# Kernel optimization log

Hardware: AMD Instinct MI355X
Metric: run time of the kernel (lower is better)

The kernel has to match this reference:

```python
import jax, jax.numpy as jnp
import numpy as np

B, LQ, LK, D = 4, 2048, 2048, 1024
H = 16  # num_heads == num_kv_heads (only runnable config of the source module)
HD = D // H  # 64


def setup_inputs() -> dict:
    key = jax.random.key(0)
    ks = jax.random.split(key, 4)
    std = 0.02
    return {
        "x": jax.random.normal(ks[0], (B, LQ, D), dtype=jnp.float32),
        "text_input": jax.random.normal(ks[1], (B, LK, D), dtype=jnp.float32),
        "Wq": jax.random.normal(ks[2], (D, D), dtype=jnp.float32) * std,
        "bq": jnp.zeros((D,), dtype=jnp.float32),
        "Wkv": jax.random.normal(ks[3], (D, 2 * D), dtype=jnp.float32) * std,
        "bkv": jnp.zeros((2 * D,), dtype=jnp.float32),
    }


def reference(x, text_input, Wq, bq, Wkv, bkv):
    b, lq, d = x.shape
    lk = text_input.shape[1]
    # projections
    Q = x @ Wq + bq                       # [b, lq, d]
    KV = text_input @ Wkv + bkv           # [b, lk, 2d]
    K, V = jnp.split(KV, 2, axis=-1)      # [b, lk, d] each
    # split heads (num_kv_heads == num_heads, so repeat_interleave is identity)
    Q = Q.reshape(b, lq, H, HD)
    K = K.reshape(b, lk, H, HD)
    V = V.reshape(b, lk, H, HD)
    # scaled dot-product attention
    scale = 1.0 / jnp.sqrt(jnp.asarray(HD, dtype=Q.dtype))
    scores = jnp.einsum("bqhd,bkhd->bhqk", Q, K) * scale  # [b, H, lq, lk]
    attn = jax.nn.softmax(scores, axis=-1)
    out = jnp.einsum("bhqk,bkhd->bqhd", attn, V)          # [b, lq, H, HD]
    # dropout p=0.0 (eval) -> identity
    return out.reshape(b, lq, d)
```

## Files before the change

kernel.cpp:

```cpp
#include <hip/hip_runtime.h>
#include <hip/hip_bf16.h>


typedef unsigned short u16;
typedef unsigned int u32;

typedef __attribute__((ext_vector_type(8))) __bf16 bf16x8;
typedef __attribute__((ext_vector_type(2))) _Float16 f16x2;
typedef __attribute__((ext_vector_type(8))) _Float16 f16x8;
typedef __attribute__((ext_vector_type(4))) float f32x4;
typedef __attribute__((ext_vector_type(16))) float f32x16;
typedef __attribute__((ext_vector_type(4))) float f4;
typedef __attribute__((ext_vector_type(4))) unsigned short u16x4;
typedef __attribute__((ext_vector_type(4))) unsigned int u32x4;

#define DEVI __device__ __forceinline__

DEVI u16 f2b(float f) {
  u32 u = __float_as_uint(f);
  return (u16)((u + 0x7fffu + ((u >> 16) & 1u)) >> 16);
}

DEVI u16 f2h(float f) {
  _Float16 h = (_Float16)f;
  return __builtin_bit_cast(u16, h);
}

DEVI f16x2 pk_f16(float a, float b) {
  return __builtin_bit_cast(f16x2, __builtin_amdgcn_cvt_pkrtz(a, b));
}

DEVI u32 cvt_pk_bf16(float a, float b) {
  u32 r;
  asm("v_cvt_pk_bf16_f32 %0, %1, %2" : "=v"(r) : "v"(a), "v"(b));
  return r;
}

DEVI void gld_lds16(void* lds, const void* g) {
  __builtin_amdgcn_global_load_lds(
      (const __attribute__((address_space(1))) u32*)g,
      (__attribute__((address_space(3))) u32*)lds, 16, 0, 0);
}

__global__ __launch_bounds__(256) void k_prep(
    const float* __restrict__ Wq, const float* __restrict__ Wkv,
    u16* __restrict__ WQT, u16* __restrict__ WKVT) {
  __shared__ float tile[32][33];
  const int bid = blockIdx.x, tid = threadIdx.x;
  const float* in;
  u16* out;
  int N, bx, by;
  if (bid < 1024) {
    in = Wq; out = WQT; N = 1024; bx = bid & 31; by = bid >> 5;
  } else {
    int b2 = bid - 1024; in = Wkv; out = WKVT; N = 2048; bx = b2 & 63; by = b2 >> 6;
  }
  const int K = 1024;
  const int n0 = bx * 32, k0 = by * 32;
  const int tx = tid & 31, ty = tid >> 5;
#pragma unroll
  for (int j = 0; j < 32; j += 8)
    tile[ty + j][tx] = in[(size_t)(k0 + ty + j) * N + n0 + tx];
  __syncthreads();
#pragma unroll
  for (int j = 0; j < 32; j += 8)
    out[(size_t)(n0 + ty + j) * K + k0 + tx] = f2b(tile[tx][ty + j]);
}

__global__ __launch_bounds__(256) void k_gemm(
    const float* __restrict__ X, const float* __restrict__ TXT,
    const u16* __restrict__ WQT, const u16* __restrict__ WKVT,
    const float* __restrict__ bq, const float* __restrict__ bkv,
    u16* __restrict__ QG, u16* __restrict__ KG, u16* __restrict__ VG) {
  __shared__ alignas(16) char As[2][8192];
  __shared__ alignas(16) char Bs[4][8192];
  const int bid0 = blockIdx.x;
  const int bid = (bid0 & 7) * 192 + (bid0 >> 3);
  const int tid = threadIdx.x;
  const int w = tid >> 6, l = tid & 63;
  const int wr = w >> 1, wc = w & 1;

  const bool isQ = bid < 512;
  int nb, mb;
  const float* Af32;
  const u16* Bptr;
  const float* bias;
  if (isQ) {
    nb = bid & 7; mb = bid >> 3; Af32 = X; Bptr = WQT; bias = bq;
  } else {
    int b2 = bid - 512; nb = b2 & 15; mb = b2 >> 4; Af32 = TXT; Bptr = WKVT; bias = bkv;
  }
  const int m0 = mb << 7, n0 = nb << 7;

  u32 doff[2], bsoff[2], fsoff[2];
#pragma unroll
  for (int i = 0; i < 2; i++) {
    u32 o = (u32)(i * 4096 + tid * 16);
    u32 row = o >> 6;
    u32 csw = (o & 63) ^ (((row >> 1) & 3) << 4);
    doff[i] = o;
    bsoff[i] = row * 2048 + csw;
    fsoff[i] = row * 4096 + 2 * csw;
  }
  const char* Abase = (const char*)Af32 + (size_t)m0 * 4096;
  const char* Borig = (const char*)Bptr + (size_t)n0 * 2048;

  f32x16 acc[2][2];
#pragma unroll
  for (int i = 0; i < 2; i++)
#pragma unroll
    for (int j = 0; j < 2; j++)
#pragma unroll
      for (int e = 0; e < 16; e++) acc[i][j][e] = 0.f;

  const u32 xk = (u32)((l >> 1) & 3);
  const u32 hi5 = (u32)(l >> 5);
  const u32 arow0 = (u32)(wr * 64 + (l & 31)) * 64;
  const u32 brow0 = (u32)(wc * 64 + (l & 31)) * 64;

  f4 sa0[4][2], sa1[4][2];

#pragma unroll
  for (int s = 0; s < 3; s++) {
#pragma unroll
    for (int i = 0; i < 2; i++) gld_lds16(&Bs[s][doff[i]], Borig + (u32)s * 64 + bsoff[i]);
#pragma unroll
    for (int i = 0; i < 2; i++) {
      sa0[s][i] = *(const f4*)(Abase + (u32)s * 128 + fsoff[i]);
      sa1[s][i] = *(const f4*)(Abase + (u32)s * 128 + fsoff[i] + 16);
    }
  }
#pragma unroll
  for (int i = 0; i < 2; i++) {
    u32x4 pk;
    pk.x = cvt_pk_bf16(sa0[0][i].x, sa0[0][i].y);
    pk.y = cvt_pk_bf16(sa0[0][i].z, sa0[0][i].w);
    pk.z = cvt_pk_bf16(sa1[0][i].x, sa1[0][i].y);
    pk.w = cvt_pk_bf16(sa1[0][i].z, sa1[0][i].w);
    *(u32x4*)&As[0][doff[i]] = pk;
  }
  asm volatile("s_waitcnt lgkmcnt(0)" ::: "memory");
  __builtin_amdgcn_s_barrier();

#define GEMM_BODY(KT, J, P)                                                        \
  do {                                                                             \
    const int kt = (KT);                                                           \
    const int S3 = ((J) + 3) & 3;                                                  \
    const int S1 = ((J) + 1) & 3;                                                  \
    if (kt < 29) { \
      _Pragma("unroll") for (int i = 0; i < 2; i++)                                \
          gld_lds16(&Bs[S3][doff[i]], Borig + (u32)(kt + 3) * 64 + bsoff[i]);      \
      _Pragma("unroll") for (int i = 0; i < 2; i++) {                              \
        sa0[S3][i] = *(const f4*)(Abase + (u32)(kt + 3) * 128 + fsoff[i]);         \
        sa1[S3][i] = *(const f4*)(Abase + (u32)(kt + 3) * 128 + fsoff[i] + 16);    \
      }                                                                            \
    }                                                                              \
    if (kt < 31) {       \
      _Pragma("unroll") for (int i = 0; i < 2; i++) {                              \
        u32x4 pk;                                                                  \
        pk.x = cvt_pk_bf16(sa0[S1][i].x, sa0[S1][i].y);                            \
        pk.y = cvt_pk_bf16(sa0[S1][i].z, sa0[S1][i].w);                            \
        pk.z = cvt_pk_bf16(sa1[S1][i].x, sa1[S1][i].y);                            \
        pk.w = cvt_pk_bf16(sa1[S1][i].z, sa1[S1][i].w);                            \
        *(u32x4*)&As[(P) ^ 1][doff[i]] = pk;                                       \
      }                                                                            \
    }                                                                              \
    bf16x8 af[2][2], bfr[2][2];                                                    \
    _Pragma("unroll") for (int i = 0; i < 2; i++)                                  \
        _Pragma("unroll") for (int h = 0; h < 2; h++) {                            \
      const u32 co = (((u32)(2 * h) + hi5) ^ xk) << 4;                             \
      af[i][h] = *(const bf16x8*)&As[(P)][arow0 + (u32)i * 2048 + co];             \
      bfr[i][h] = *(const bf16x8*)&Bs[(J)][brow0 + (u32)i * 2048 + co];            \
    }                                                                              \
    _Pragma("unroll") for (int i = 0; i < 2; i++)                                  \
        _Pragma("unroll") for (int j2 = 0; j2 < 2; j2++)                           \
            _Pragma("unroll") for (int h = 0; h < 2; h++)                          \
                acc[i][j2] = __builtin_amdgcn_mfma_f32_32x32x16_bf16(              \
                    af[i][h], bfr[j2][h], acc[i][j2], 0, 0, 0);                    \
    asm volatile("s_waitcnt lgkmcnt(0)" ::: "memory");                             \
    __builtin_amdgcn_s_barrier();                                                  \
  } while (0)

  for (int k4 = 0; k4 < 8; k4++) {
    const int kt0 = k4 * 4;
    GEMM_BODY(kt0 + 0, 0, 0);
    GEMM_BODY(kt0 + 1, 1, 1);
    GEMM_BODY(kt0 + 2, 2, 0);
    GEMM_BODY(kt0 + 3, 3, 1);
  }
#undef GEMM_BODY

#pragma unroll
  for (int i = 0; i < 2; i++)
#pragma unroll
    for (int j = 0; j < 2; j++) {
      const int n = n0 + wc * 64 + j * 32 + (l & 31);
      const float bv = bias[n];
#pragma unroll
      for (int rg = 0; rg < 4; rg++) {
        const int mbase = m0 + wr * 64 + i * 32 + rg * 8 + ((l >> 5) << 2);
        const int bb = mbase >> 11;
        const int mrow = mbase & 2047;
        float a0 = acc[i][j][rg * 4 + 0] + bv;
        float a1 = acc[i][j][rg * 4 + 1] + bv;
        float a2 = acc[i][j][rg * 4 + 2] + bv;
        float a3 = acc[i][j][rg * 4 + 3] + bv;
        if (isQ) {
          const int h = n >> 6, hd = n & 63;
          u16* dst = QG + ((((size_t)bb * 16 + h) * 2048 + mrow) << 6) + hd;
          dst[0] = f2b(a0 * 0.18033688011112042f);
          dst[64] = f2b(a1 * 0.18033688011112042f);
          dst[128] = f2b(a2 * 0.18033688011112042f);
          dst[192] = f2b(a3 * 0.18033688011112042f);
        } else if (n < 1024) {
          const int h = n >> 6, d = n & 63;
          char* base = (char*)KG + ((((size_t)bb * 16 + h) * 2048 + mrow) << 7);
          float av[4] = {a0, a1, a2, a3};
#pragma unroll
          for (int r = 0; r < 4; r++) {
            u32 off = (u32)r * 128 + (((u32)d * 2) ^ (((u32)(mrow + r) & 7) << 4));
            *(u16*)(base + off) = f2b(av[r]);
          }
        } else {
          const int nn = n - 1024;
          const int h = nn >> 6, hd = nn & 63;
          u16x4 pk;
          pk.x = f2h(a0); pk.y = f2h(a1); pk.z = f2h(a2); pk.w = f2h(a3);
          char* base = (char*)VG + (((size_t)bb * 16 + h) << 18);
          u32 off = ((u32)(mrow >> 6) << 13) + (((u32)(mrow >> 5) & 1) << 12) +
                    ((u32)(hd >> 4) << 10) + (((u32)(mrow >> 2) & 3) << 8) +
                    ((u32)(hd & 15) << 4) + (((u32)(mrow >> 4) & 1) << 3);
          *(u16x4*)(base + off) = pk;
        }
      }
    }
}

__global__ __launch_bounds__(256) void k_attn(
    const u16* __restrict__ QG, const u16* __restrict__ KG, const u16* __restrict__ VG,
    float* __restrict__ out) {
  __shared__ alignas(16) char Ks[2][8192];
  __shared__ alignas(16) char Vs[2][8192];
  const int tid = threadIdx.x, w = tid >> 6, l = tid & 63;
  const int g = l >> 4, q = l & 15;
  const int bid = blockIdx.x;
  const int orig = (bid & 7) * 128 + (bid >> 3);
  const int qt = orig & 15;
  const int hh = (orig >> 4) & 15;
  const int b = orig >> 8;
  const size_t bh = (size_t)b * 16 + hh;

  const int qrowA = qt * 128 + w * 16 + q;
  const int qrowB = qrowA + 64;

  const u16* QpA = QG + ((bh * 2048 + (size_t)qrowA) << 6) + (g << 3);
  const u16* QpB = QG + ((bh * 2048 + (size_t)qrowB) << 6) + (g << 3);
  const bf16x8 qf0a = *(const bf16x8*)QpA;
  const bf16x8 qf1a = *(const bf16x8*)(QpA + 32);
  const bf16x8 qf0b = *(const bf16x8*)QpB;
  const bf16x8 qf1b = *(const bf16x8*)(QpB + 32);

  const char* Kbase = (const char*)KG + (bh << 18);
  const char* Vbase = (const char*)VG + (bh << 18);

  f32x4 lsA = (f32x4){0.f, 0.f, 0.f, 0.f};
  f32x4 lsB = (f32x4){0.f, 0.f, 0.f, 0.f};
  f32x4 oa[4], ob4[4];
#pragma unroll
  for (int c = 0; c < 4; c++) {
    oa[c] = (f32x4){0.f, 0.f, 0.f, 0.f};
    ob4[c] = (f32x4){0.f, 0.f, 0.f, 0.f};
  }
  f16x8 ones8;
#pragma unroll
  for (int e = 0; e < 8; e++) ones8[e] = (_Float16)1.0f;

  gld_lds16(&Ks[0][tid * 16], Kbase + tid * 16);
  gld_lds16(&Ks[0][4096 + tid * 16], Kbase + 4096 + tid * 16);
  gld_lds16(&Vs[0][tid * 16], Vbase + tid * 16);
  gld_lds16(&Vs[0][4096 + tid * 16], Vbase + 4096 + tid * 16);
  __syncthreads();

  const u32 ksw = ((u32)(l & 7)) << 4;
  const u32 kro = ((u32)q) << 7;
  const u32 kin = ((u32)g) << 4;

  auto body = [&](int BUF, int kb) {
    if (kb < 31) {
      const char* kp = Kbase + (size_t)(kb + 1) * 8192 + tid * 16;
      const char* vp = Vbase + (size_t)(kb + 1) * 8192 + tid * 16;
      gld_lds16(&Ks[BUF ^ 1][tid * 16], kp);
      gld_lds16(&Ks[BUF ^ 1][4096 + tid * 16], kp + 4096);
      gld_lds16(&Vs[BUF ^ 1][tid * 16], vp);
      gld_lds16(&Vs[BUF ^ 1][4096 + tid * 16], vp + 4096);
    }
    f32x4 sa[4], sb[4];
    __builtin_amdgcn_s_setprio(1);
#pragma unroll
    for (int t = 0; t < 4; t++) {
      const char* kr = &Ks[BUF][kro + (u32)t * 2048];
      bf16x8 kf0 = *(const bf16x8*)(kr + (kin ^ ksw));
      bf16x8 kf1 = *(const bf16x8*)(kr + ((kin + 64) ^ ksw));
      f32x4 z = (f32x4){0.f, 0.f, 0.f, 0.f};
      sa[t] = __builtin_amdgcn_mfma_f32_16x16x32_bf16(kf0, qf0a, z, 0, 0, 0);
      sa[t] = __builtin_amdgcn_mfma_f32_16x16x32_bf16(kf1, qf1a, sa[t], 0, 0, 0);
      sb[t] = __builtin_amdgcn_mfma_f32_16x16x32_bf16(kf0, qf0b, z, 0, 0, 0);
      sb[t] = __builtin_amdgcn_mfma_f32_16x16x32_bf16(kf1, qf1b, sb[t], 0, 0, 0);
    }
    __builtin_amdgcn_s_setprio(0);

    float pA[4][4], pB[4][4];
#pragma unroll
    for (int t = 0; t < 4; t++)
#pragma unroll
      for (int r = 0; r < 4; r++) {
        pA[t][r] = __builtin_amdgcn_exp2f(sa[t][r]);
        pB[t][r] = __builtin_amdgcn_exp2f(sb[t][r]);
      }

    __builtin_amdgcn_s_setprio(1);
#pragma unroll
    for (int u = 0; u < 2; u++) {
      f16x2 a0 = pk_f16(pA[2 * u][0], pA[2 * u][1]);
      f16x2 a1 = pk_f16(pA[2 * u][2], pA[2 * u][3]);
      f16x2 a2 = pk_f16(pA[2 * u + 1][0], pA[2 * u + 1][1]);
      f16x2 a3 = pk_f16(pA[2 * u + 1][2], pA[2 * u + 1][3]);
      f16x8 pfa;
      pfa[0] = a0.x; pfa[1] = a0.y; pfa[2] = a1.x; pfa[3] = a1.y;
      pfa[4] = a2.x; pfa[5] = a2.y; pfa[6] = a3.x; pfa[7] = a3.y;
      f16x2 b0 = pk_f16(pB[2 * u][0], pB[2 * u][1]);
      f16x2 b1 = pk_f16(pB[2 * u][2], pB[2 * u][3]);
      f16x2 b2 = pk_f16(pB[2 * u + 1][0], pB[2 * u + 1][1]);
      f16x2 b3 = pk_f16(pB[2 * u + 1][2], pB[2 * u + 1][3]);
      f16x8 pfb;
      pfb[0] = b0.x; pfb[1] = b0.y; pfb[2] = b1.x; pfb[3] = b1.y;
      pfb[4] = b2.x; pfb[5] = b2.y; pfb[6] = b3.x; pfb[7] = b3.y;
      lsA = __builtin_amdgcn_mfma_f32_16x16x32_f16(ones8, pfa, lsA, 0, 0, 0);
      lsB = __builtin_amdgcn_mfma_f32_16x16x32_f16(ones8, pfb, lsB, 0, 0, 0);
#pragma unroll
      for (int c = 0; c < 4; c++) {
        f16x8 vf = *(const f16x8*)&Vs[BUF][(u32)u * 4096 + (u32)c * 1024 + (u32)l * 16];
        oa[c] = __builtin_amdgcn_mfma_f32_16x16x32_f16(vf, pfa, oa[c], 0, 0, 0);
        ob4[c] = __builtin_amdgcn_mfma_f32_16x16x32_f16(vf, pfb, ob4[c], 0, 0, 0);
      }
    }
    __builtin_amdgcn_s_setprio(0);
    __syncthreads();
  };

  for (int kb2 = 0; kb2 < 16; kb2++) {
    body(0, 2 * kb2);
    body(1, 2 * kb2 + 1);
  }

  const float invA = 1.0f / lsA.x;
  const float invB = 1.0f / lsB.x;
  float* obA = out + ((size_t)b * 2048 + (size_t)qrowA) * 1024 + hh * 64;
  float* obB = out + ((size_t)b * 2048 + (size_t)qrowB) * 1024 + hh * 64;
#pragma unroll
  for (int c = 0; c < 4; c++) {
    f32x4 va = oa[c] * invA;
    f32x4 vb2 = ob4[c] * invB;
    *(f32x4*)(obA + c * 16 + g * 4) = va;
    *(f32x4*)(obB + c * 16 + g * 4) = vb2;
  }
}

extern "C" void kernel_launch(void* const* d_in, const int* in_sizes, int n_in,
                              void* d_out, int out_size, void* d_ws, size_t ws_size,
                              hipStream_t stream) {
  const float* x = (const float*)d_in[0];
  const float* text = (const float*)d_in[1];
  const float* Wq = (const float*)d_in[2];
  const float* bq = (const float*)d_in[3];
  const float* Wkv = (const float*)d_in[4];
  const float* bkv = (const float*)d_in[5];
  float* out = (float*)d_out;
  char* ws = (char*)d_ws;

  const size_t MiB = 1u << 20;
  u16* WQT = (u16*)(ws + 0 * MiB);
  u16* WKVT = (u16*)(ws + 2 * MiB);
  u16* QG = (u16*)(ws + 6 * MiB);
  u16* KG = (u16*)(ws + 22 * MiB);
  u16* VG = (u16*)(ws + 38 * MiB);

  k_prep<<<3072, 256, 0, stream>>>(Wq, Wkv, WQT, WKVT);
  k_gemm<<<1536, 256, 0, stream>>>(x, text, WQT, WKVT, bq, bkv, QG, KG, VG);
  k_attn<<<1024, 256, 0, stream>>>(QG, KG, VG, out);
}
```

Baseline: 162.7 us.

## Widen GEMM tile to 128x256 and switch to simple double buffering

The projection GEMM tile grows from 128x128 to 128x256, so each wave computes 2x4 MFMA accumulators, more work reuses each A tile, and the grid is halved to 768 blocks. The deep 4-stage B ring and 3-deep register prefetch of A are replaced by a 2-stage double buffer. Each step now waits on vmcnt(0) before its barrier, and A conversion is deferred until after the MFMAs. This aims to cut global and LDS traffic per FLOP, at the cost of shallower latency hiding, more accumulator registers (lower occupancy), and fewer blocks to spread over the CUs.

```diff
diff --git a/kernel.cpp b/kernel.cpp
--- a/kernel.cpp
+++ b/kernel.cpp
@@ -73,149 +73,155 @@
     const float* __restrict__ bq, const float* __restrict__ bkv,
     u16* __restrict__ QG, u16* __restrict__ KG, u16* __restrict__ VG) {
   __shared__ alignas(16) char As[2][8192];
-  __shared__ alignas(16) char Bs[4][8192];
+  __shared__ alignas(16) char Bs[2][16384];
   const int bid0 = blockIdx.x;
-  const int bid = (bid0 & 7) * 192 + (bid0 >> 3);
+  const int bid = (bid0 & 7) * 96 + (bid0 >> 3);
   const int tid = threadIdx.x;
   const int w = tid >> 6, l = tid & 63;
   const int wr = w >> 1, wc = w & 1;
 
-  const bool isQ = bid < 512;
+  const bool isQ = bid < 256;
   int nb, mb;
   const float* Af32;
   const u16* Bptr;
   const float* bias;
   if (isQ) {
-    nb = bid & 7; mb = bid >> 3; Af32 = X; Bptr = WQT; bias = bq;
+    nb = bid & 3; mb = bid >> 2; Af32 = X; Bptr = WQT; bias = bq;
   } else {
-    int b2 = bid - 512; nb = b2 & 15; mb = b2 >> 4; Af32 = TXT; Bptr = WKVT; bias = bkv;
-  }
-  const int m0 = mb << 7, n0 = nb << 7;
-
-  u32 doff[2], bsoff[2], fsoff[2];
+    int b2 = bid - 256; nb = b2 & 7; mb = b2 >> 3; Af32 = TXT; Bptr = WKVT; bias = bkv;
+  }
+  const int m0 = mb << 7, n0 = nb << 8;
+
+  u32 doffA[2], fsoff[2];
+  u32 doffB[4], bsoff[4];
 #pragma unroll
   for (int i = 0; i < 2; i++) {
     u32 o = (u32)(i * 4096 + tid * 16);
     u32 row = o >> 6;
     u32 csw = (o & 63) ^ (((row >> 1) & 3) << 4);
-    doff[i] = o;
-    bsoff[i] = row * 2048 + csw;
+    doffA[i] = o;
     fsoff[i] = row * 4096 + 2 * csw;
+  }
+#pragma unroll
+  for (int j = 0; j < 4; j++) {
+    u32 o = (u32)(j * 4096 + tid * 16);
+    u32 row = o >> 6;
+    u32 csw = (o & 63) ^ (((row >> 1) & 3) << 4);
+    doffB[j] = o;
+    bsoff[j] = row * 2048 + csw;
   }
   const char* Abase = (const char*)Af32 + (size_t)m0 * 4096;
   const char* Borig = (const char*)Bptr + (size_t)n0 * 2048;
 
-  f32x16 acc[2][2];
+  f32x16 acc[2][4];
 #pragma unroll
   for (int i = 0; i < 2; i++)
 #pragma unroll
-    for (int j = 0; j < 2; j++)
+    for (int j = 0; j < 4; j++)
 #pragma unroll
       for (int e = 0; e < 16; e++) acc[i][j][e] = 0.f;
 
   const u32 xk = (u32)((l >> 1) & 3);
   const u32 hi5 = (u32)(l >> 5);
   const u32 arow0 = (u32)(wr * 64 + (l & 31)) * 64;
-  const u32 brow0 = (u32)(wc * 64 + (l & 31)) * 64;
-
-  f4 sa0[4][2], sa1[4][2];
-
-#pragma unroll
-  for (int s = 0; s < 3; s++) {
-#pragma unroll
-    for (int i = 0; i < 2; i++) gld_lds16(&Bs[s][doff[i]], Borig + (u32)s * 64 + bsoff[i]);
-#pragma unroll
-    for (int i = 0; i < 2; i++) {
-      sa0[s][i] = *(const f4*)(Abase + (u32)s * 128 + fsoff[i]);
-      sa1[s][i] = *(const f4*)(Abase + (u32)s * 128 + fsoff[i] + 16);
-    }
+  const u32 brow0 = (u32)(wc * 128 + (l & 31)) * 64;
+
+  f4 a0[2], a1[2];
+
+#pragma unroll
+  for (int j = 0; j < 4; j++) gld_lds16(&Bs[0][doffB[j]], Borig + bsoff[j]);
+#pragma unroll
+  for (int i = 0; i < 2; i++) {
+    a0[i] = *(const f4*)(Abase + fsoff[i]);
+    a1[i] = *(const f4*)(Abase + fsoff[i] + 16);
   }
 #pragma unroll
   for (int i = 0; i < 2; i++) {
     u32x4 pk;
-    pk.x = cvt_pk_bf16(sa0[0][i].x, sa0[0][i].y);
-    pk.y = cvt_pk_bf16(sa0[0][i].z, sa0[0][i].w);
-    pk.z = cvt_pk_bf16(sa1[0][i].x, sa1[0][i].y);
-    pk.w = cvt_pk_bf16(sa1[0][i].z, sa1[0][i].w);
-    *(u32x4*)&As[0][doff[i]] = pk;
-  }
-  asm volatile("s_waitcnt lgkmcnt(0)" ::: "memory");
+    pk.x = cvt_pk_bf16(a0[i].x, a0[i].y);
+    pk.y = cvt_pk_bf16(a0[i].z, a0[i].w);
+    pk.z = cvt_pk_bf16(a1[i].x, a1[i].y);
+    pk.w = cvt_pk_bf16(a1[i].z, a1[i].w);
+    *(u32x4*)&As[0][doffA[i]] = pk;
+  }
+  asm volatile("s_waitcnt vmcnt(0) lgkmcnt(0)" ::: "memory");
   __builtin_amdgcn_s_barrier();
 
-#define GEMM_BODY(KT, J, P)                                                        \
+#define GEMM_BODY(KT, BUF)                                                         \
   do {                                                                             \
     const int kt = (KT);                                                           \
-    const int S3 = ((J) + 3) & 3;                                                  \
-    const int S1 = ((J) + 1) & 3;                                                  \
-    if (kt < 29) { \
-      _Pragma("unroll") for (int i = 0; i < 2; i++)                                \
-          gld_lds16(&Bs[S3][doff[i]], Borig + (u32)(kt + 3) * 64 + bsoff[i]);      \
+    if (kt < 31) {     \
+      _Pragma("unroll") for (int j = 0; j < 4; j++)                                \
+          gld_lds16(&Bs[(BUF) ^ 1][doffB[j]],                                      \
+                    Borig + (u32)(kt + 1) * 64 + bsoff[j]);                        \
       _Pragma("unroll") for (int i = 0; i < 2; i++) {                              \
-        sa0[S3][i] = *(const f4*)(Abase + (u32)(kt + 3) * 128 + fsoff[i]);         \
-        sa1[S3][i] = *(const f4*)(Abase + (u32)(kt + 3) * 128 + fsoff[i] + 16);    \
+        a0[i] = *(const f4*)(Abase + (u32)(kt + 1) * 128 + fsoff[i]);              \
+        a1[i] = *(const f4*)(Abase + (u32)(kt + 1) * 128 + fsoff[i] + 16);         \
       }                                                                            \
     }                                                                              \
-    if (kt < 31) {       \
-      _Pragma("unroll") for (int i = 0; i < 2; i++) {                              \
-        u32x4 pk;                                                                  \
-        pk.x = cvt_pk_bf16(sa0[S1][i].x, sa0[S1][i].y);                            \
-        pk.y = cvt_pk_bf16(sa0[S1][i].z, sa0[S1][i].w);                            \
-        pk.z = cvt_pk_bf16(sa1[S1][i].x, sa1[S1][i].y);                            \
-        pk.w = cvt_pk_bf16(sa1[S1][i].z, sa1[S1][i].w);                            \
-        *(u32x4*)&As[(P) ^ 1][doff[i]] = pk;                                       \
-      }                                                                            \
-    }                                                                              \
-    bf16x8 af[2][2], bfr[2][2];                                                    \
+    bf16x8 af[2][2];                                                               \
     _Pragma("unroll") for (int i = 0; i < 2; i++)                                  \
         _Pragma("unroll") for (int h = 0; h < 2; h++) {                            \
       const u32 co = (((u32)(2 * h) + hi5) ^ xk) << 4;                             \
-      af[i][h] = *(const bf16x8*)&As[(P)][arow0 + (u32)i * 2048 + co];             \
-      bfr[i][h] = *(const bf16x8*)&Bs[(J)][brow0 + (u32)i * 2048 + co];            \
+      af[i][h] = *(const bf16x8*)&As[(BUF)][arow0 + (u32)i * 2048 + co];           \
     }                                                                              \
-    _Pragma("unroll") for (int i = 0; i < 2; i++)                                  \
-        _Pragma("unroll") for (int j2 = 0; j2 < 2; j2++)                           \
-            _Pragma("unroll") for (int h = 0; h < 2; h++)                          \
-                acc[i][j2] = __builtin_amdgcn_mfma_f32_32x32x16_bf16(              \
-                    af[i][h], bfr[j2][h], acc[i][j2], 0, 0, 0);                    \
-    asm volatile("s_waitcnt lgkmcnt(0)" ::: "memory");                             \
+    _Pragma("unroll") for (int j2 = 0; j2 < 4; j2++) {                             \
+      bf16x8 bf[2];                                                                \
+      _Pragma("unroll") for (int h = 0; h < 2; h++) {                              \
+        const u32 co = (((u32)(2 * h) + hi5) ^ xk) << 4;                           \
+        bf[h] = *(const bf16x8*)&Bs[(BUF)][brow0 + (u32)j2 * 2048 + co];           \
+      }                                                                            \
+      _Pragma("unroll") for (int i = 0; i < 2; i++)                                \
+          _Pragma("unroll") for (int h = 0; h < 2; h++)                            \
+              acc[i][j2] = __builtin_amdgcn_mfma_f32_32x32x16_bf16(                \
+                  af[i][h], bf[h], acc[i][j2], 0, 0, 0);                           \
+    }                                                                              \
+    if (kt < 31) {                                \
+      _Pragma("unroll") for (int i = 0; i < 2; i++) {                              \
+        u32x4 pk;                                                                  \
+        pk.x = cvt_pk_bf16(a0[i].x, a0[i].y);                                      \
+        pk.y = cvt_pk_bf16(a0[i].z, a0[i].w);                                      \
+        pk.z = cvt_pk_bf16(a1[i].x, a1[i].y);                                      \
+        pk.w = cvt_pk_bf16(a1[i].z, a1[i].w);                                      \
+        *(u32x4*)&As[(BUF) ^ 1][doffA[i]] = pk;                                    \
+      }                                                                            \
+    }                                                                              \
+    asm volatile("s_waitcnt vmcnt(0) lgkmcnt(0)" ::: "memory");                    \
     __builtin_amdgcn_s_barrier();                                                  \
   } while (0)
 
-  for (int k4 = 0; k4 < 8; k4++) {
-    const int kt0 = k4 * 4;
-    GEMM_BODY(kt0 + 0, 0, 0);
-    GEMM_BODY(kt0 + 1, 1, 1);
-    GEMM_BODY(kt0 + 2, 2, 0);
-    GEMM_BODY(kt0 + 3, 3, 1);
+  for (int k2 = 0; k2 < 16; k2++) {
+    GEMM_BODY(2 * k2, 0);
+    GEMM_BODY(2 * k2 + 1, 1);
   }
 #undef GEMM_BODY
 
 #pragma unroll
   for (int i = 0; i < 2; i++)
 #pragma unroll
-    for (int j = 0; j < 2; j++) {
-      const int n = n0 + wc * 64 + j * 32 + (l & 31);
+    for (int j = 0; j < 4; j++) {
+      const int n = n0 + wc * 128 + j * 32 + (l & 31);
       const float bv = bias[n];
 #pragma unroll
       for (int rg = 0; rg < 4; rg++) {
         const int mbase = m0 + wr * 64 + i * 32 + rg * 8 + ((l >> 5) << 2);
         const int bb = mbase >> 11;
         const int mrow = mbase & 2047;
-        float a0 = acc[i][j][rg * 4 + 0] + bv;
-        float a1 = acc[i][j][rg * 4 + 1] + bv;
-        float a2 = acc[i][j][rg * 4 + 2] + bv;
-        float a3 = acc[i][j][rg * 4 + 3] + bv;
+        float a0e = acc[i][j][rg * 4 + 0] + bv;
+        float a1e = acc[i][j][rg * 4 + 1] + bv;
+        float a2e = acc[i][j][rg * 4 + 2] + bv;
+        float a3e = acc[i][j][rg * 4 + 3] + bv;
         if (isQ) {
           const int h = n >> 6, hd = n & 63;
           u16* dst = QG + ((((size_t)bb * 16 + h) * 2048 + mrow) << 6) + hd;
-          dst[0] = f2b(a0 * 0.18033688011112042f);
-          dst[64] = f2b(a1 * 0.18033688011112042f);
-          dst[128] = f2b(a2 * 0.18033688011112042f);
-          dst[192] = f2b(a3 * 0.18033688011112042f);
+          dst[0] = f2b(a0e * 0.18033688011112042f);
+          dst[64] = f2b(a1e * 0.18033688011112042f);
+          dst[128] = f2b(a2e * 0.18033688011112042f);
+          dst[192] = f2b(a3e * 0.18033688011112042f);
         } else if (n < 1024) {
           const int h = n >> 6, d = n & 63;
           char* base = (char*)KG + ((((size_t)bb * 16 + h) * 2048 + mrow) << 7);
-          float av[4] = {a0, a1, a2, a3};
+          float av[4] = {a0e, a1e, a2e, a3e};
 #pragma unroll
           for (int r = 0; r < 4; r++) {
             u32 off = (u32)r * 128 + (((u32)d * 2) ^ (((u32)(mrow + r) & 7) << 4));
@@ -225,7 +231,7 @@
           const int nn = n - 1024;
           const int h = nn >> 6, hd = nn & 63;
           u16x4 pk;
-          pk.x = f2h(a0); pk.y = f2h(a1); pk.z = f2h(a2); pk.w = f2h(a3);
+          pk.x = f2h(a0e); pk.y = f2h(a1e); pk.z = f2h(a2e); pk.w = f2h(a3e);
           char* base = (char*)VG + (((size_t)bb * 16 + h) << 18);
           u32 off = ((u32)(mrow >> 6) << 13) + (((u32)(mrow >> 5) & 1) << 12) +
                     ((u32)(hd >> 4) << 10) + (((u32)(mrow >> 2) & 3) << 8) +
@@ -386,6 +392,6 @@
   u16* VG = (u16*)(ws + 38 * MiB);
 
   k_prep<<<3072, 256, 0, stream>>>(Wq, Wkv, WQT, WKVT);
-  k_gemm<<<1536, 256, 0, stream>>>(x, text, WQT, WKVT, bq, bkv, QG, KG, VG);
+  k_gemm<<<768, 256, 0, stream>>>(x, text, WQT, WKVT, bq, bkv, QG, KG, VG);
   k_attn<<<1024, 256, 0, stream>>>(QG, KG, VG, out);
 }
```

New measurement: 169.8 us. 1.04x slower.
